# Optimization experiments

Measured on AMD Instinct MI355X. Metric: run time of the kernel, lower is better.

Reference implementation:

```python
import jax, jax.numpy as jnp
import numpy as np

PATCH = 3  # patch_size, padding = PATCH//2 = 1, stride = 1
EPS = 1e-12  # F.normalize eps


def extract_patches(x):
    """F.unfold(k=3, stride=1, pad=1) then reshape to [B, N, C, 3, 3] (N=H*W)."""
    b, c, h, w = x.shape
    xp = jnp.pad(x, ((0, 0), (0, 0), (1, 1), (1, 1)))
    # stack the 9 shifted views: [B, C, 9, H, W]; order (kh, kw) matches torch unfold
    shifts = [xp[:, :, i:i + h, j:j + w] for i in range(PATCH) for j in range(PATCH)]
    p = jnp.stack(shifts, axis=2)
    p = p.reshape(b, c, PATCH, PATCH, h * w)
    return jnp.transpose(p, (0, 4, 1, 2, 3))  # [B, N, C, 3, 3]


def cosine_similarity(x, y):
    """x, y: [B, N, ...] patch sets -> [B, Nx, Ny] cosine similarity."""
    b = x.shape[0]
    xf = x.reshape(b, x.shape[1], -1)
    yf = y.reshape(b, y.shape[1], -1)
    xn = xf / jnp.maximum(jnp.linalg.norm(xf, axis=2, keepdims=True), EPS)
    yn = yf / jnp.maximum(jnp.linalg.norm(yf, axis=2, keepdims=True), EPS)
    return jnp.einsum('bnd,bmd->bnm', xn, yn)


def setup_inputs() -> dict:
    key = jax.random.key(0)
    k1, k2, k3, k4 = jax.random.split(key, 4)
    B, C, H, W = 2, 64, 80, 80
    return {
        'content_feat': jax.random.normal(k1, (B, C, H, W), dtype=jnp.float32),
        'style_feat': jax.random.normal(k2, (B, C, H, W), dtype=jnp.float32),
        'content_mask': jax.random.uniform(k3, (B, 3, H, W), dtype=jnp.float32),
        'style_mask': jax.random.uniform(k4, (B, 3, H, W), dtype=jnp.float32),
    }


def reference(content_feat, style_feat, content_mask, style_mask):
    content_patches = extract_patches(content_feat)      # [B, N, C, 3, 3]
    style_patches = extract_patches(style_feat)          # [B, N, C, 3, 3]
    cmask_patches = extract_patches(content_mask)        # [B, N, 3, 3, 3]
    smask_patches = extract_patches(style_mask)          # [B, N, 3, 3, 3]

    feat_sim = cosine_similarity(content_patches, style_patches)   # [B, N, N]
    mask_sim = cosine_similarity(cmask_patches, smask_patches)     # [B, N, N]
    similarity = feat_sim * mask_sim

    best = jnp.argmax(similarity, axis=2)                # [B, N]
    b, n = best.shape
    sp_flat = style_patches.reshape(b, n, -1)            # [B, N, C*9]
    matched = jnp.take_along_axis(sp_flat, best[:, :, None], axis=1)
    return matched.reshape(style_patches.shape)          # [B, N, C, 3, 3]
```

## Files before the change

kernel.cpp:

```cpp
#include <hip/hip_runtime.h>

#define HH 80
#define WW 80
#define NPIX 6400
#define PW 82
#define NPP (PW*PW)
#define CFE 64
#define CMA 3
#define KF 576
#define GUARD 1024
#define NREG 8

#define PA 1024
#define POUT 856
#define BW 1056

typedef unsigned long long u64;
typedef unsigned int u32;

__device__ __forceinline__ void gload4(const float* g, float* l) {
    __builtin_amdgcn_global_load_lds((const __attribute__((address_space(1))) void*)g,
                                     (__attribute__((address_space(3))) void*)l, 4, 0, 0);
}
__device__ __forceinline__ float4 ld4(const float* p) { return *(const float4*)p; }

__global__ __launch_bounds__(256)
void pixsq_kernel(const float* __restrict__ sf, const float* __restrict__ sm,
                  float* __restrict__ psf, float* __restrict__ psm) {
    int g = blockIdx.x * 256 + threadIdx.x;
    if (g >= 2 * NPIX) return;
    int b = g / NPIX, m = g - b * NPIX;
    const float* p = sf + (size_t)b * CFE * NPIX + m;
    float a = 0.f;
    #pragma unroll 8
    for (int c = 0; c < CFE; ++c) { float v = p[c * NPIX]; a = fmaf(v, v, a); }
    const float* q = sm + (size_t)b * CMA * NPIX + m;
    float am = 0.f;
    #pragma unroll
    for (int c = 0; c < CMA; ++c) { float v = q[c * NPIX]; am = fmaf(v, v, am); }
    psf[g] = a; psm[g] = am;
}

__global__ __launch_bounds__(256)
void rn2_kernel(const float* __restrict__ psf, const float* __restrict__ psm,
                float* __restrict__ rn2p) {
    int g = blockIdx.x * 256 + threadIdx.x;
    if (g >= 2 * NPIX) return;
    int b = g / NPIX, m = g - b * NPIX;
    int mh = m / WW, mw = m - mh * WW;
    float sF = 0.f, sM = 0.f;
    #pragma unroll
    for (int di = -1; di <= 1; ++di) {
        if ((unsigned)(mh + di) >= HH) continue;
        #pragma unroll
        for (int dj = -1; dj <= 1; ++dj) {
            if ((unsigned)(mw + dj) >= WW) continue;
            int mm = m + di * WW + dj;
            sF += psf[b * NPIX + mm];
            sM += psm[b * NPIX + mm];
        }
    }
    float rf = 1.f / fmaxf(sqrtf(sF), 1e-12f);
    float rm = 1.f / fmaxf(sqrtf(sM), 1e-12f);
    rn2p[(size_t)b * NPP + (mh + 1) * PW + (mw + 1)] = rf * rm;
}

__global__ __launch_bounds__(256)
void pad_kernel(const float* __restrict__ cf, const float* __restrict__ sf,
                const float* __restrict__ cm, const float* __restrict__ sm,
                float* __restrict__ cfp, float* __restrict__ sfp,
                float* __restrict__ cmp, float* __restrict__ smp) {
    int gid = blockIdx.x * 256 + threadIdx.x;
    if (gid >= 2 * 2 * 67 * NPIX) return;
    int pix = gid % NPIX; int t = gid / NPIX;
    int c = t % 67; t /= 67;
    int b = t & 1; int which = t >> 1;
    int h = pix / WW, w = pix - h * WW;
    int qq = (h + 1) * PW + (w + 1);
    if (which == 0) {
        if (c < 64) cfp[((size_t)b * CFE + c) * NPP + qq] = cf[((size_t)b * CFE + c) * NPIX + pix];
        else        cmp[((size_t)b * CMA + (c - 64)) * NPP + qq] = cm[((size_t)b * CMA + (c - 64)) * NPIX + pix];
    } else {
        if (c < 64) sfp[((size_t)b * CFE + c) * NPP + qq] = sf[((size_t)b * CFE + c) * NPIX + pix];
        else        smp[((size_t)b * CMA + (c - 64)) * NPP + qq] = sm[((size_t)b * CMA + (c - 64)) * NPIX + pix];
    }
}

__global__ __launch_bounds__(512, 2)
void fuse_kernel(const float* __restrict__ cfp, const float* __restrict__ sfp,
                 const float* __restrict__ cmp, const float* __restrict__ smp,
                 const float* __restrict__ rn2p, u64* __restrict__ pbest) {
    const int pt = blockIdx.y;
    const int b  = blockIdx.z;
    const int pstart = 83 + POUT * pt;
    const int pend   = min(pstart + POUT, 6641);
    const int pbase  = pstart - 84;
    const int dte0   = (6644 - pend) >> 5;
    const int dtemax = (13200 - pstart) >> 5;
    const int dte = dte0 + blockIdx.x;
    if (dte > dtemax) return;
    const int d0 = -6560 + 32 * dte;

    __shared__ float pool[PA * 36];

    const int tid = threadIdx.x;
    const int tp = tid & 255;
    const int tg = tid >> 8;
    const int wb = tid & 448;
    const int swz = (tp & 7) << 2;

    const float* cfb = cfp + (size_t)b * CFE * NPP + pbase;
    const float* sfb = sfp + (size_t)b * CFE * NPP + pbase + d0;
    const float* cmb = cmp + (size_t)b * CMA * NPP + pbase;
    const float* smb = smp + (size_t)b * CMA * NPP + pbase + d0;

    float acc[4][16];
    float pdF[2][32], pdM[2][32];

    auto zacc = [&]() {
        #pragma unroll
        for (int k = 0; k < 4; ++k)
            #pragma unroll
            for (int j = 0; j < 16; ++j) acc[k][j] = 0.f;
    };

    auto stageF = [&](int q, int buf) {
        float* Ab = pool + buf * 16640;
        float* Bb = Ab + 8 * PA;
        const float* As = cfb + (size_t)(q * 8) * NPP;
        const float* Bs = sfb + (size_t)(q * 8) * NPP;
        #pragma unroll
        for (int cc = 0; cc < 8; ++cc) {
            gload4(As + cc * NPP + tid,       Ab + cc * PA + wb);
            gload4(As + cc * NPP + 512 + tid, Ab + cc * PA + 512 + wb);
            gload4(Bs + cc * NPP + tid,       Bb + cc * BW + wb);
            gload4(Bs + cc * NPP + 512 + tid, Bb + cc * BW + 512 + wb);
            if (tid < 32) gload4(Bs + cc * NPP + 1024 + tid, Bb + cc * BW + 1024);
        }
    };

    auto gemmc = [&](const float* Ab, const float* Bb) {
        const float* Ar = Ab + 4 * tp;
        const float* Br = Bb + 4 * tp + 16 * tg;
        float a[4], bb[20];
        *(float4*)a         = ld4(Ar);
        *(float4*)bb        = ld4(Br);
        *(float4*)(bb + 4)  = ld4(Br + 4);
        *(float4*)(bb + 8)  = ld4(Br + 8);
        *(float4*)(bb + 12) = ld4(Br + 12);
        *(float4*)(bb + 16) = ld4(Br + 16);
        #pragma unroll
        for (int k = 0; k < 4; ++k)
            #pragma unroll
            for (int j = 0; j < 16; ++j)
                acc[k][j] = fmaf(a[k], bb[k + j], acc[k][j]);
    };

    auto s0write = [&]() {
        #pragma unroll
        for (int k = 0; k < 4; ++k) {
            float* dr = pool + (4 * tp + k) * 36;
            #pragma unroll
            for (int g = 0; g < 4; ++g) {
                *(float4*)(dr + ((16 * tg + 4 * g) ^ swz)) =
                    make_float4(acc[k][4 * g], acc[k][4 * g + 1],
                                acc[k][4 * g + 2], acc[k][4 * g + 3]);
            }
        }
    };

    auto tapsrun = [&](float (&pd)[2][32]) {
        #pragma unroll
        for (int s = 0; s < 2; ++s) {
            const int row = tid + 512 * s;
            if (row < 84 || row >= 84 + POUT) continue;
            #pragma unroll
            for (int j4 = 0; j4 < 8; ++j4) {
                float4 v = make_float4(0.f, 0.f, 0.f, 0.f);
                #pragma unroll
                for (int t9 = 0; t9 < 9; ++t9) {
                    static const int dlt[9] = {-83, -82, -81, -1, 0, 1, 81, 82, 83};
                    const int rr = row + dlt[t9];
                    const int sw = ((rr >> 2) & 7) << 2;
                    float4 t = ld4(pool + rr * 36 + ((4 * j4) ^ sw));
                    v.x += t.x; v.y += t.y; v.z += t.z; v.w += t.w;
                }
                pd[s][4 * j4 + 0] = v.x; pd[s][4 * j4 + 1] = v.y;
                pd[s][4 * j4 + 2] = v.z; pd[s][4 * j4 + 3] = v.w;
            }
        }
    };

    zacc();
    stageF(0, 0);
    __syncthreads();
    int buf = 0;
    #pragma unroll 1
    for (int q = 0; q < 8; ++q) {
        if (q < 7) stageF(q + 1, buf ^ 1);
        const float* Ab = pool + buf * 16640;
        const float* Bb = Ab + 8 * PA;
        #pragma unroll 2
        for (int cc = 0; cc < 8; ++cc)
            gemmc(Ab + cc * PA, Bb + cc * BW);
        __syncthreads();
        buf ^= 1;
    }
    s0write();
    __syncthreads();
    tapsrun(pdF);
    __syncthreads();

    #pragma unroll
    for (int cc = 0; cc < 3; ++cc) {
        gload4(cmb + cc * NPP + tid,       pool + cc * PA + wb);
        gload4(cmb + cc * NPP + 512 + tid, pool + cc * PA + 512 + wb);
        gload4(smb + cc * NPP + tid,       pool + 3 * PA + cc * BW + wb);
        gload4(smb + cc * NPP + 512 + tid, pool + 3 * PA + cc * BW + 512 + wb);
        if (tid < 32) gload4(smb + cc * NPP + 1024 + tid, pool + 3 * PA + cc * BW + 1024);
    }
    __syncthreads();
    zacc();
    #pragma unroll
    for (int cc = 0; cc < 3; ++cc)
        gemmc(pool + cc * PA, pool + 3 * PA + cc * BW);
    __syncthreads();
    s0write();
    __syncthreads();
    tapsrun(pdM);

    const float* rb = rn2p + (size_t)b * NPP;
    u64* pb = pbest + ((size_t)(dte & (NREG - 1)) * 2 + b) * NPIX;
    #pragma unroll
    for (int s = 0; s < 2; ++s) {
        const int row = tid + 512 * s;
        const int p = pbase + row;
        if (row < 84 || p >= pend) continue;
        int ph = p / PW, pw2 = p - ph * PW;
        if (ph < 1 || ph > 80 || pw2 < 1 || pw2 > 80) continue;
        int n_real = (ph - 1) * 80 + (pw2 - 1);
        u64 key = 0;
        #pragma unroll
        for (int j = 0; j < 32; ++j) {
            int mp = p + d0 + j;
            if ((unsigned)mp >= (unsigned)NPP) continue;
            float r2 = rb[mp];
            if (r2 == 0.f) continue;
            float sc = pdF[s][j] * pdM[s][j] * r2;
            sc += 0.f;
            u32 u = __float_as_uint(sc);
            u ^= (u >> 31) ? 0xFFFFFFFFu : 0x80000000u;
            u64 k2 = ((u64)u << 32) | (u32)~(u32)mp;
            if (k2 > key) key = k2;
        }
        if (key) {
            u64 cur = pb[n_real];
            if (key > cur) atomicMax(&pb[n_real], key);
        }
    }
}

__global__ __launch_bounds__(64)
void gather_kernel(const float* __restrict__ sf, const u64* __restrict__ pbest,
                   float* __restrict__ out) {
    int n = blockIdx.x, b = blockIdx.y;
    int lane = threadIdx.x;

    u64 key = 0;
    #pragma unroll
    for (int r = 0; r < NREG; ++r) {
        u64 k = pbest[((size_t)r * 2 + b) * NPIX + n];
        if (k > key) key = k;
    }
    int mp = (int)(~(u32)key);
    int m = 0;
    if ((unsigned)mp < (unsigned)NPP) {
        int ph = mp / PW, pw = mp - ph * PW;
        if (ph >= 1 && ph <= 80 && pw >= 1 && pw <= 80)
            m = (ph - 1) * 80 + (pw - 1);
    }
    int mh = m / WW, mw = m - mh * WW;
    const float* sfb = sf + (size_t)b * CFE * NPIX;
    float* ob = out + ((size_t)b * NPIX + n) * (size_t)KF;
    #pragma unroll
    for (int e = lane; e < KF; e += 64) {
        int c = e / 9, pos = e - c * 9;
        int di = pos / 3 - 1, dj = pos - (pos / 3) * 3 - 1;
        int h = mh + di, w = mw + dj;
        ob[e] = ((unsigned)h < HH && (unsigned)w < WW) ? sfb[c * NPIX + h * WW + w] : 0.f;
    }
}

extern "C" void kernel_launch(void* const* d_in, const int* in_sizes, int n_in,
                              void* d_out, int out_size, void* d_ws, size_t ws_size,
                              hipStream_t stream) {
    const float* cf = (const float*)d_in[0];
    const float* sf = (const float*)d_in[1];
    const float* cm = (const float*)d_in[2];
    const float* sm = (const float*)d_in[3];
    float* out = (float*)d_out;

    float* psf = (float*)d_ws;
    float* psm = psf + 2 * NPIX;
    u64*  pbest = (u64*)(psm + 2 * NPIX);
    float* rn2p = (float*)(pbest + (size_t)NREG * 2 * NPIX);
    float* padreg = rn2p + 2 * NPP;
    float* cfp = padreg + GUARD;
    float* sfp = cfp + (size_t)2 * CFE * NPP + GUARD;
    float* cmp = sfp + (size_t)2 * CFE * NPP + GUARD;
    float* smp = cmp + (size_t)2 * CMA * NPP + GUARD;

    size_t zero_bytes = (size_t)NREG * 2 * NPIX * 8 +
        ((size_t)2 * NPP + (size_t)5 * GUARD +
         (size_t)4 * CFE * NPP + (size_t)4 * CMA * NPP) * 4;
    hipMemsetAsync(pbest, 0, zero_bytes, stream);

    pad_kernel<<<(2 * 2 * 67 * NPIX + 255) / 256, 256, 0, stream>>>(
        cf, sf, cm, sm, cfp, sfp, cmp, smp);
    pixsq_kernel<<<(2 * NPIX + 255) / 256, 256, 0, stream>>>(sf, sm, psf, psm);
    rn2_kernel  <<<(2 * NPIX + 255) / 256, 256, 0, stream>>>(psf, psm, rn2p);

    fuse_kernel<<<dim3(232, 8, 2), 512, 0, stream>>>(cfp, sfp, cmp, smp, rn2p, pbest);

    gather_kernel<<<dim3(NPIX, 2), 64, 0, stream>>>(sf, pbest, out);
}
```

Baseline: 684.4 us.

## Restructure fuse kernel to 1024 threads with register-resident A operand

The fused similarity kernel now runs 1024 threads per block, and each thread computes a 4x8 tile instead of 4x16. The content (A) operand is read straight from global memory into registers with software prefetch, and only the style (B) operand is staged in LDS. The 3x3 tap summation is rewritten with a sliding window over rows, and the per-pixel argmax keys are combined with wave shuffles before the atomic. The aim is to raise occupancy, cut register pressure and LDS traffic, and reduce redundant tap loads. The cost is uncoalesced-looking global A loads, since each thread reads a float4 at stride 4, and more threads contending at barriers.

```diff
diff --git a/kernel.cpp b/kernel.cpp
--- a/kernel.cpp
+++ b/kernel.cpp
@@ -17,6 +17,8 @@
 
 typedef unsigned long long u64;
 typedef unsigned int u32;
+
+struct f4u { float x, y, z, w; };
 
 __device__ __forceinline__ void gload4(const float* g, float* l) {
     __builtin_amdgcn_global_load_lds((const __attribute__((address_space(1))) void*)g,
@@ -86,7 +88,7 @@
     }
 }
 
-__global__ __launch_bounds__(512, 2)
+__global__ __launch_bounds__(1024, 4)
 void fuse_kernel(const float* __restrict__ cfp, const float* __restrict__ sfp,
                  const float* __restrict__ cmp, const float* __restrict__ smp,
                  const float* __restrict__ rn2p, u64* __restrict__ pbest) {
@@ -106,53 +108,45 @@
     const int tid = threadIdx.x;
     const int tp = tid & 255;
     const int tg = tid >> 8;
-    const int wb = tid & 448;
+    const int wb = tid & 960;
     const int swz = (tp & 7) << 2;
 
-    const float* cfb = cfp + (size_t)b * CFE * NPP + pbase;
-    const float* sfb = sfp + (size_t)b * CFE * NPP + pbase + d0;
-    const float* cmb = cmp + (size_t)b * CMA * NPP + pbase;
-    const float* smb = smp + (size_t)b * CMA * NPP + pbase + d0;
-
-    float acc[4][16];
-    float pdF[2][32], pdM[2][32];
+    const float* Aglob = cfp + (size_t)b * CFE * NPP + pbase + 4 * tp;
+    const float* Bglob = sfp + (size_t)b * CFE * NPP + pbase + d0;
+    const float* AglobM = cmp + (size_t)b * CMA * NPP + pbase + 4 * tp;
+    const float* BglobM = smp + (size_t)b * CMA * NPP + pbase + d0;
+
+    float acc[4][8];
+    float pdF[8][4], pdM[8][4];
 
     auto zacc = [&]() {
         #pragma unroll
         for (int k = 0; k < 4; ++k)
             #pragma unroll
-            for (int j = 0; j < 16; ++j) acc[k][j] = 0.f;
-    };
-
-    auto stageF = [&](int q, int buf) {
-        float* Ab = pool + buf * 16640;
-        float* Bb = Ab + 8 * PA;
-        const float* As = cfb + (size_t)(q * 8) * NPP;
-        const float* Bs = sfb + (size_t)(q * 8) * NPP;
+            for (int j = 0; j < 8; ++j) acc[k][j] = 0.f;
+    };
+
+    auto stageB = [&](int q, int buf) {
+        float* Bb = pool + buf * (8 * BW);
+        const float* Bs = Bglob + (size_t)(q * 8) * NPP;
         #pragma unroll
         for (int cc = 0; cc < 8; ++cc) {
-            gload4(As + cc * NPP + tid,       Ab + cc * PA + wb);
-            gload4(As + cc * NPP + 512 + tid, Ab + cc * PA + 512 + wb);
-            gload4(Bs + cc * NPP + tid,       Bb + cc * BW + wb);
-            gload4(Bs + cc * NPP + 512 + tid, Bb + cc * BW + 512 + wb);
+            gload4(Bs + cc * NPP + tid, Bb + cc * BW + wb);
             if (tid < 32) gload4(Bs + cc * NPP + 1024 + tid, Bb + cc * BW + 1024);
         }
     };
 
-    auto gemmc = [&](const float* Ab, const float* Bb) {
-        const float* Ar = Ab + 4 * tp;
-        const float* Br = Bb + 4 * tp + 16 * tg;
-        float a[4], bb[20];
-        *(float4*)a         = ld4(Ar);
-        *(float4*)bb        = ld4(Br);
-        *(float4*)(bb + 4)  = ld4(Br + 4);
-        *(float4*)(bb + 8)  = ld4(Br + 8);
-        *(float4*)(bb + 12) = ld4(Br + 12);
-        *(float4*)(bb + 16) = ld4(Br + 16);
+    auto gemmc1 = [&](const f4u& a4, const float* Bb) {
+        const float* Br = Bb + 4 * tp + 8 * tg;
+        float bb[12];
+        *(float4*)bb       = ld4(Br);
+        *(float4*)(bb + 4) = ld4(Br + 4);
+        *(float4*)(bb + 8) = ld4(Br + 8);
+        const float a[4] = {a4.x, a4.y, a4.z, a4.w};
         #pragma unroll
         for (int k = 0; k < 4; ++k)
             #pragma unroll
-            for (int j = 0; j < 16; ++j)
+            for (int j = 0; j < 8; ++j)
                 acc[k][j] = fmaf(a[k], bb[k + j], acc[k][j]);
     };
 
@@ -160,102 +154,120 @@
         #pragma unroll
         for (int k = 0; k < 4; ++k) {
             float* dr = pool + (4 * tp + k) * 36;
-            #pragma unroll
-            for (int g = 0; g < 4; ++g) {
-                *(float4*)(dr + ((16 * tg + 4 * g) ^ swz)) =
-                    make_float4(acc[k][4 * g], acc[k][4 * g + 1],
-                                acc[k][4 * g + 2], acc[k][4 * g + 3]);
+            *(float4*)(dr + ((8 * tg) ^ swz)) =
+                make_float4(acc[k][0], acc[k][1], acc[k][2], acc[k][3]);
+            *(float4*)(dr + ((8 * tg + 4) ^ swz)) =
+                make_float4(acc[k][4], acc[k][5], acc[k][6], acc[k][7]);
+        }
+    };
+
+    auto tapsrun = [&](float (&pd)[8][4]) {
+        if (tid >= 856) return;
+        const int rg = tid >> 3, dg = tid & 7;
+        const int p0w = 84 + 8 * rg;
+        #pragma unroll
+        for (int k = 0; k < 8; ++k)
+            #pragma unroll
+            for (int j = 0; j < 4; ++j) pd[k][j] = 0.f;
+        static const int dg3[3] = {-82, 0, 82};
+        #pragma unroll
+        for (int g = 0; g < 3; ++g) {
+            float4 w[10];
+            #pragma unroll
+            for (int r = 0; r < 10; ++r) {
+                const int rr = p0w + dg3[g] - 1 + r;
+                const int sw = ((rr >> 2) & 7) << 2;
+                w[r] = ld4(pool + rr * 36 + ((4 * dg) ^ sw));
             }
-        }
-    };
-
-    auto tapsrun = [&](float (&pd)[2][32]) {
-        #pragma unroll
-        for (int s = 0; s < 2; ++s) {
-            const int row = tid + 512 * s;
-            if (row < 84 || row >= 84 + POUT) continue;
-            #pragma unroll
-            for (int j4 = 0; j4 < 8; ++j4) {
-                float4 v = make_float4(0.f, 0.f, 0.f, 0.f);
-                #pragma unroll
-                for (int t9 = 0; t9 < 9; ++t9) {
-                    static const int dlt[9] = {-83, -82, -81, -1, 0, 1, 81, 82, 83};
-                    const int rr = row + dlt[t9];
-                    const int sw = ((rr >> 2) & 7) << 2;
-                    float4 t = ld4(pool + rr * 36 + ((4 * j4) ^ sw));
-                    v.x += t.x; v.y += t.y; v.z += t.z; v.w += t.w;
-                }
-                pd[s][4 * j4 + 0] = v.x; pd[s][4 * j4 + 1] = v.y;
-                pd[s][4 * j4 + 2] = v.z; pd[s][4 * j4 + 3] = v.w;
+            #pragma unroll
+            for (int k = 0; k < 8; ++k) {
+                pd[k][0] += w[k].x + w[k + 1].x + w[k + 2].x;
+                pd[k][1] += w[k].y + w[k + 1].y + w[k + 2].y;
+                pd[k][2] += w[k].z + w[k + 1].z + w[k + 2].z;
+                pd[k][3] += w[k].w + w[k + 1].w + w[k + 2].w;
             }
         }
     };
 
     zacc();
-    stageF(0, 0);
-    __syncthreads();
-    int buf = 0;
+    f4u A0[4], A1[4];
+    #pragma unroll
+    for (int c = 0; c < 4; ++c) A0[c] = *(const f4u*)(Aglob + (size_t)c * NPP);
+    stageB(0, 0);
+    __syncthreads();
     #pragma unroll 1
     for (int q = 0; q < 8; ++q) {
-        if (q < 7) stageF(q + 1, buf ^ 1);
-        const float* Ab = pool + buf * 16640;
-        const float* Bb = Ab + 8 * PA;
-        #pragma unroll 2
-        for (int cc = 0; cc < 8; ++cc)
-            gemmc(Ab + cc * PA, Bb + cc * BW);
+        const int buf = q & 1;
+        if (q < 7) stageB(q + 1, buf ^ 1);
+        #pragma unroll
+        for (int c = 0; c < 4; ++c) A1[c] = *(const f4u*)(Aglob + (size_t)(q * 8 + 4 + c) * NPP);
+        const float* Bb = pool + buf * (8 * BW);
+        #pragma unroll
+        for (int c = 0; c < 4; ++c) gemmc1(A0[c], Bb + c * BW);
+        if (q < 7) {
+            #pragma unroll
+            for (int c = 0; c < 4; ++c) A0[c] = *(const f4u*)(Aglob + (size_t)((q + 1) * 8 + c) * NPP);
+        }
+        #pragma unroll
+        for (int c = 0; c < 4; ++c) gemmc1(A1[c], Bb + (4 + c) * BW);
         __syncthreads();
-        buf ^= 1;
     }
     s0write();
     __syncthreads();
     tapsrun(pdF);
     __syncthreads();
 
-    #pragma unroll
-    for (int cc = 0; cc < 3; ++cc) {
-        gload4(cmb + cc * NPP + tid,       pool + cc * PA + wb);
-        gload4(cmb + cc * NPP + 512 + tid, pool + cc * PA + 512 + wb);
-        gload4(smb + cc * NPP + tid,       pool + 3 * PA + cc * BW + wb);
-        gload4(smb + cc * NPP + 512 + tid, pool + 3 * PA + cc * BW + 512 + wb);
-        if (tid < 32) gload4(smb + cc * NPP + 1024 + tid, pool + 3 * PA + cc * BW + 1024);
+    f4u Am[3];
+    #pragma unroll
+    for (int c = 0; c < 3; ++c) {
+        Am[c] = *(const f4u*)(AglobM + (size_t)c * NPP);
+        gload4(BglobM + (size_t)c * NPP + tid, pool + c * BW + wb);
+        if (tid < 32) gload4(BglobM + (size_t)c * NPP + 1024 + tid, pool + c * BW + 1024);
     }
     __syncthreads();
     zacc();
     #pragma unroll
-    for (int cc = 0; cc < 3; ++cc)
-        gemmc(pool + cc * PA, pool + 3 * PA + cc * BW);
+    for (int c = 0; c < 3; ++c) gemmc1(Am[c], pool + c * BW);
     __syncthreads();
     s0write();
     __syncthreads();
     tapsrun(pdM);
 
-    const float* rb = rn2p + (size_t)b * NPP;
-    u64* pb = pbest + ((size_t)(dte & (NREG - 1)) * 2 + b) * NPIX;
-    #pragma unroll
-    for (int s = 0; s < 2; ++s) {
-        const int row = tid + 512 * s;
-        const int p = pbase + row;
-        if (row < 84 || p >= pend) continue;
-        int ph = p / PW, pw2 = p - ph * PW;
-        if (ph < 1 || ph > 80 || pw2 < 1 || pw2 > 80) continue;
-        int n_real = (ph - 1) * 80 + (pw2 - 1);
-        u64 key = 0;
-        #pragma unroll
-        for (int j = 0; j < 32; ++j) {
-            int mp = p + d0 + j;
-            if ((unsigned)mp >= (unsigned)NPP) continue;
-            float r2 = rb[mp];
-            if (r2 == 0.f) continue;
-            float sc = pdF[s][j] * pdM[s][j] * r2;
-            sc += 0.f;
-            u32 u = __float_as_uint(sc);
-            u ^= (u >> 31) ? 0xFFFFFFFFu : 0x80000000u;
-            u64 k2 = ((u64)u << 32) | (u32)~(u32)mp;
-            if (k2 > key) key = k2;
-        }
-        if (key) {
-            u64 cur = pb[n_real];
-            if (key > cur) atomicMax(&pb[n_real], key);
+    if (tid < 856) {
+        const int rg = tid >> 3, dg = tid & 7;
+        const float* rb = rn2p + (size_t)b * NPP;
+        u64* pb = pbest + ((size_t)(dte & (NREG - 1)) * 2 + b) * NPIX;
+        #pragma unroll
+        for (int k = 0; k < 8; ++k) {
+            const int row = 84 + 8 * rg + k;
+            const int p = pbase + row;
+            const int ph = p / PW, pw2 = p - ph * PW;
+            const bool ok = (p < pend) && (ph >= 1) && (ph <= 80) && (pw2 >= 1) && (pw2 <= 80);
+            u64 key = 0;
+            if (ok) {
+                #pragma unroll
+                for (int j = 0; j < 4; ++j) {
+                    int mp = p + d0 + 4 * dg + j;
+                    if ((unsigned)mp >= (unsigned)NPP) continue;
+                    float r2 = rb[mp];
+                    if (r2 == 0.f) continue;
+                    float sc = pdF[k][j] * pdM[k][j] * r2;
+                    sc += 0.f;
+                    u32 u = __float_as_uint(sc);
+                    u ^= (u >> 31) ? 0xFFFFFFFFu : 0x80000000u;
+                    u64 k2 = ((u64)u << 32) | (u32)~(u32)mp;
+                    if (k2 > key) key = k2;
+                }
+            }
+            u64 o;
+            o = __shfl_xor(key, 1); if (o > key) key = o;
+            o = __shfl_xor(key, 2); if (o > key) key = o;
+            o = __shfl_xor(key, 4); if (o > key) key = o;
+            if (dg == 0 && key) {
+                const int n_real = (ph - 1) * 80 + (pw2 - 1);
+                u64 cur = pb[n_real];
+                if (key > cur) atomicMax(&pb[n_real], key);
+            }
         }
     }
 }
@@ -320,7 +332,7 @@
     pixsq_kernel<<<(2 * NPIX + 255) / 256, 256, 0, stream>>>(sf, sm, psf, psm);
     rn2_kernel  <<<(2 * NPIX + 255) / 256, 256, 0, stream>>>(psf, psm, rn2p);
 
-    fuse_kernel<<<dim3(232, 8, 2), 512, 0, stream>>>(cfp, sfp, cmp, smp, rn2p, pbest);
+    fuse_kernel<<<dim3(232, 8, 2), 1024, 0, stream>>>(cfp, sfp, cmp, smp, rn2p, pbest);
 
     gather_kernel<<<dim3(NPIX, 2), 64, 0, stream>>>(sf, pbest, out);
 }
```

Result: slower. 1.012 ms (+47.9%).
